# Performance work log

Measured on AMD Instinct MI355X. Metric: run time of the kernel, lower is better.

The kernel has to match this reference:

```python
import jax, jax.numpy as jnp
import numpy as np

B, D, R = 8192, 4096, 64
REG_W, REG_C = 0.01, 0.05


def setup_inputs() -> dict:
    key = jax.random.key(0)
    ks = jax.random.split(key, 7)
    return {
        "X": jax.random.normal(ks[0], (B, D), dtype=jnp.float32),
        "U1": jax.random.normal(ks[1], (1, D, R), dtype=jnp.float32),
        "U2": jax.random.normal(ks[2], (2, D, R), dtype=jnp.float32),
        "U3": jax.random.normal(ks[3], (3, D, R), dtype=jnp.float32),
        "C": jax.random.normal(ks[4], (3,), dtype=jnp.float32),
        "beta": jax.random.normal(ks[5], (1,), dtype=jnp.float32),
        "C_sin": jax.random.normal(ks[6], (1,), dtype=jnp.float32),
    }


def reference(X, U1, U2, U3, C, beta, C_sin):
    # term_j(x) = sum_r prod_{i<=j} <x, U_j[i, :, r]>
    result = jnp.broadcast_to(beta[0], (X.shape[0],))
    reg_loss_w = jnp.float32(0.0)
    for j, U in enumerate((U1, U2, U3)):
        dots = jnp.einsum("bd,odr->obr", X, U)      # [order, B, R]
        term = jnp.prod(dots, axis=0).sum(axis=1)   # [B]
        result = result + C[j] * term
        reg_loss_w = reg_loss_w + REG_W * (jnp.abs(U).sum() / U.size)
    sine_term = C_sin[0] * jnp.sin(X).sum(axis=1)
    result = result + sine_term
    reg_loss_c = REG_C * (jnp.abs(C).sum() + jnp.abs(C_sin).sum())
    total_reg = reg_loss_w + reg_loss_c
    return result, total_reg
```

## Files before the change

### kernel.cpp

```cpp
#include <hip/hip_runtime.h>
#include <hip/hip_bf16.h>

typedef float f32x4 __attribute__((ext_vector_type(4)));
typedef short s16x8 __attribute__((ext_vector_type(8)));

#define D_DIM 4096
#define NT 24
#define BM 128
#define NBODY 32
#define BOFF 0
#define AOFF 49152
#define SINW_OFF 3145728u
#define PART_OFF 3276800u

__device__ __forceinline__ unsigned short f2bf(float f) {
    unsigned u = __float_as_uint(f);
    u += 0x7fffu + ((u >> 16) & 1u);
    return (unsigned short)(u >> 16);
}

__device__ __forceinline__ void gload16(const void* g, void* l) {
    __builtin_amdgcn_global_load_lds(
        (const __attribute__((address_space(1))) unsigned int*)g,
        (__attribute__((address_space(3))) unsigned int*)l, 16, 0, 0);
}

__global__ __launch_bounds__(64) void reg_init_kernel(const float* __restrict__ C,
                                                      const float* __restrict__ Csin,
                                                      float* __restrict__ reg_out) {
    if (threadIdx.x == 0)
        reg_out[0] = 0.05f * (fabsf(C[0]) + fabsf(C[1]) + fabsf(C[2]) + fabsf(Csin[0]));
}

__global__ __launch_bounds__(64) void build_w_kernel(const float* __restrict__ U1,
                                                     const float* __restrict__ U2,
                                                     const float* __restrict__ U3,
                                                     unsigned short* __restrict__ W,
                                                     float* __restrict__ reg_out) {
    const int ks = blockIdx.x / NT;
    const int ct = blockIdx.x % NT;
    const int l  = threadIdx.x;
    const int n  = ct * 16 + (l & 15);
    const int kb = ks * 32 + ((l >> 4) << 3);

    const float* src;
    float scale;
    if (n < 64)       { src = U1 + n;                  scale = 0.01f / 262144.f; }
    else if (n < 128) { src = U2 + (n - 64);           scale = 0.01f / 524288.f; }
    else if (n < 192) { src = U2 + 262144 + (n - 128); scale = 0.01f / 524288.f; }
    else if (n < 256) { src = U3 + (n - 192);          scale = 0.01f / 786432.f; }
    else if (n < 320) { src = U3 + 262144 + (n - 256); scale = 0.01f / 786432.f; }
    else              { src = U3 + 524288 + (n - 320); scale = 0.01f / 786432.f; }

    unsigned short h[8];
    float sabs = 0.f;
#pragma unroll
    for (int j = 0; j < 8; ++j) {
        float u = src[(size_t)(kb + j) * 64];
        sabs += fabsf(u);
        h[j] = f2bf(u);
    }
    uint4 pk;
    pk.x = (unsigned)h[0] | ((unsigned)h[1] << 16);
    pk.y = (unsigned)h[2] | ((unsigned)h[3] << 16);
    pk.z = (unsigned)h[4] | ((unsigned)h[5] << 16);
    pk.w = (unsigned)h[6] | ((unsigned)h[7] << 16);
    *(uint4*)(W + ((size_t)blockIdx.x * 64 + l) * 8) = pk;

    sabs *= scale;
#pragma unroll
    for (int off = 32; off >= 1; off >>= 1)
        sabs += __shfl_xor(sabs, off, 64);
    if (l == 0) atomicAdd(reg_out, sabs);
}

__global__ __launch_bounds__(1024, 4) void poly_main_kernel(const float* __restrict__ X,
                                                            const unsigned short* __restrict__ W,
                                                            _Float16* __restrict__ part,
                                                            float* __restrict__ sinws) {
    __shared__ __align__(16) char pool[65536];

    const int t    = threadIdx.x;
    const int lane = t & 63;
    const int wv   = t >> 6;
    const int rg   = wv >> 3;
    const int cg   = wv & 7;
    const int ct0  = cg * 3;
    const int rb   = blockIdx.x >> 2;
    const int ks   = blockIdx.x & 3;
    const int row0 = rb * BM;

    const int sr = t >> 3;
    const int k4 = (t & 7) << 2;
    const float* xp = X + (size_t)(row0 + sr) * D_DIM + ks * 1024 + k4;
    const int awfrag = (sr >> 4) * 1024
                     + ((((k4 >> 3) << 4) | (sr & 15)) * 16) + ((k4 & 7) << 1);

    const int nB  = (wv < 8) ? 2 : 1;
    const int ch0 = (wv < 8) ? (wv * 2) : (wv + 8);
    const int slab0 = ks * 32;

    f32x4 acc00{}, acc01{}, acc02{}, acc10{}, acc11{}, acc12{},
          acc20{}, acc21{}, acc22{}, acc30{}, acc31{}, acc32{};
    float sinacc = 0.f;

#define STAGE(bufl, XV)                                                         \
    {                                                                           \
        sinacc += __sinf(XV.x) + __sinf(XV.y) + __sinf(XV.z) + __sinf(XV.w);    \
        uint2 h_;                                                               \
        h_.x = (unsigned)f2bf(XV.x) | ((unsigned)f2bf(XV.y) << 16);             \
        h_.y = (unsigned)f2bf(XV.z) | ((unsigned)f2bf(XV.w) << 16);             \
        *(uint2*)(pool + AOFF + (bufl) * 8192 + awfrag) = h_;                   \
    }

    {
        const unsigned short* g0 = W + (size_t)slab0 * 12288 + ch0 * 512 + lane * 8;
        gload16(g0, pool + BOFF + ch0 * 1024);
        if (nB == 2) gload16(g0 + 512, pool + BOFF + (ch0 + 1) * 1024);
    }
    f32x4 xn;
    {
        f32x4 x0 = *(const f32x4*)xp;
        STAGE(0, x0);
        xn = *(const f32x4*)(xp + 32);
    }
    asm volatile("s_waitcnt lgkmcnt(0)" ::: "memory");
    asm volatile("s_waitcnt vmcnt(1)" ::: "memory");
    __builtin_amdgcn_s_barrier();
    __builtin_amdgcn_sched_barrier(0);

#define BODY(d_, CUR, NXT)                                                      \
    {                                                                           \
        const int d__ = (d_);                                                   \
        if (d__ + 1 < NBODY) {                                                  \
            const unsigned short* g_ = W + (size_t)(slab0 + d__ + 1) * 12288    \
                                         + ch0 * 512 + lane * 8;                \
            gload16(g_, pool + BOFF + (NXT) * 24576 + ch0 * 1024);              \
            if (nB == 2)                                                        \
                gload16(g_ + 512, pool + BOFF + (NXT) * 24576 + (ch0 + 1) * 1024);\
        }                                                                       \
        int sl_ = d__ + 2; if (sl_ > NBODY - 1) sl_ = NBODY - 1;                \
        f32x4 xf_ = *(const f32x4*)(xp + (size_t)sl_ * 32);                     \
        if (d__ + 1 < NBODY) { STAGE(NXT, xn); }                                \
        xn = xf_;                                                               \
        const char* ab_ = pool + AOFF + (CUR) * 8192;                           \
        const char* bb_ = pool + BOFF + (CUR) * 24576;                          \
        s16x8 af0_ = *(const s16x8*)(ab_ + (rg * 4 + 0) * 1024 + lane * 16);    \
        s16x8 af1_ = *(const s16x8*)(ab_ + (rg * 4 + 1) * 1024 + lane * 16);    \
        s16x8 af2_ = *(const s16x8*)(ab_ + (rg * 4 + 2) * 1024 + lane * 16);    \
        s16x8 af3_ = *(const s16x8*)(ab_ + (rg * 4 + 3) * 1024 + lane * 16);    \
        s16x8 bf0_ = *(const s16x8*)(bb_ + (ct0 + 0) * 1024 + lane * 16);       \
        s16x8 bf1_ = *(const s16x8*)(bb_ + (ct0 + 1) * 1024 + lane * 16);       \
        s16x8 bf2_ = *(const s16x8*)(bb_ + (ct0 + 2) * 1024 + lane * 16);       \
        asm volatile("s_waitcnt lgkmcnt(0)" ::: "memory");                      \
        __builtin_amdgcn_sched_barrier(0);                                      \
        __builtin_amdgcn_s_setprio(1);                                          \
        acc00 = __builtin_amdgcn_mfma_f32_16x16x32_bf16(af0_, bf0_, acc00, 0, 0, 0); \
        acc01 = __builtin_amdgcn_mfma_f32_16x16x32_bf16(af0_, bf1_, acc01, 0, 0, 0); \
        acc02 = __builtin_amdgcn_mfma_f32_16x16x32_bf16(af0_, bf2_, acc02, 0, 0, 0); \
        acc10 = __builtin_amdgcn_mfma_f32_16x16x32_bf16(af1_, bf0_, acc10, 0, 0, 0); \
        acc11 = __builtin_amdgcn_mfma_f32_16x16x32_bf16(af1_, bf1_, acc11, 0, 0, 0); \
        acc12 = __builtin_amdgcn_mfma_f32_16x16x32_bf16(af1_, bf2_, acc12, 0, 0, 0); \
        acc20 = __builtin_amdgcn_mfma_f32_16x16x32_bf16(af2_, bf0_, acc20, 0, 0, 0); \
        acc21 = __builtin_amdgcn_mfma_f32_16x16x32_bf16(af2_, bf1_, acc21, 0, 0, 0); \
        acc22 = __builtin_amdgcn_mfma_f32_16x16x32_bf16(af2_, bf2_, acc22, 0, 0, 0); \
        acc30 = __builtin_amdgcn_mfma_f32_16x16x32_bf16(af3_, bf0_, acc30, 0, 0, 0); \
        acc31 = __builtin_amdgcn_mfma_f32_16x16x32_bf16(af3_, bf1_, acc31, 0, 0, 0); \
        acc32 = __builtin_amdgcn_mfma_f32_16x16x32_bf16(af3_, bf2_, acc32, 0, 0, 0); \
        __builtin_amdgcn_s_setprio(0);                                          \
        asm volatile("s_waitcnt vmcnt(1)" ::: "memory");                        \
        __builtin_amdgcn_s_barrier();                                           \
        __builtin_amdgcn_sched_barrier(0);                                      \
    }

    for (int d = 0; d < NBODY; d += 2) {
        BODY(d, 0, 1);
        BODY(d + 1, 1, 0);
    }
#undef BODY
#undef STAGE

    _Float16* pb = part + (size_t)ks * 8192 * 384;
    const int lr4 = (lane >> 4) << 2;
    const int lc  = lane & 15;
    const f32x4 accA[4][3] = {{acc00, acc01, acc02}, {acc10, acc11, acc12},
                              {acc20, acc21, acc22}, {acc30, acc31, acc32}};
#pragma unroll
    for (int rf = 0; rf < 4; ++rf)
#pragma unroll
        for (int c = 0; c < 3; ++c) {
            const int col = (ct0 + c) * 16 + lc;
#pragma unroll
            for (int i = 0; i < 4; ++i) {
                const int rl = rg * 64 + rf * 16 + lr4 + i;
                pb[(size_t)(row0 + rl) * 384 + col] = (_Float16)accA[rf][c][i];
            }
        }

    sinacc += __shfl_xor(sinacc, 1);
    sinacc += __shfl_xor(sinacc, 2);
    sinacc += __shfl_xor(sinacc, 4);
    if ((t & 7) == 0)
        sinws[(size_t)ks * 8192 + row0 + sr] = sinacc;
}

__global__ __launch_bounds__(512) void combine_kernel(const _Float16* __restrict__ part,
                                                      const float* __restrict__ sinws,
                                                      const float* __restrict__ C,
                                                      const float* __restrict__ beta,
                                                      const float* __restrict__ Csin,
                                                      float* __restrict__ out) {
    const int t   = threadIdx.x;
    const int row = blockIdx.x * 32 + (t >> 4);
    const int cc  = t & 15;
    const size_t rbase = (size_t)row * 384;

    float t1 = 0.f, t2 = 0.f, t3 = 0.f;
#pragma unroll
    for (int j = 0; j < 4; ++j) {
        const int c = j * 16 + cc;
        float a1 = 0.f, a2 = 0.f, b2 = 0.f, a3 = 0.f, b3 = 0.f, c3 = 0.f;
#pragma unroll
        for (int q = 0; q < 4; ++q) {
            const _Float16* p = part + (size_t)q * 8192 * 384 + rbase;
            a1 += (float)p[c];
            a2 += (float)p[64 + c];
            b2 += (float)p[128 + c];
            a3 += (float)p[192 + c];
            b3 += (float)p[256 + c];
            c3 += (float)p[320 + c];
        }
        t1 += a1;
        t2 += a2 * b2;
        t3 += a3 * b3 * c3;
    }
#pragma unroll
    for (int off = 1; off < 16; off <<= 1) {
        t1 += __shfl_xor(t1, off, 16);
        t2 += __shfl_xor(t2, off, 16);
        t3 += __shfl_xor(t3, off, 16);
    }
    if (cc == 0) {
        const float s = sinws[row] + sinws[8192 + row]
                      + sinws[2 * 8192 + row] + sinws[3 * 8192 + row];
        out[row] = beta[0] + C[0] * t1 + C[1] * t2 + C[2] * t3 + Csin[0] * s;
    }
}

extern "C" void kernel_launch(void* const* d_in, const int* in_sizes, int n_in,
                              void* d_out, int out_size, void* d_ws, size_t ws_size,
                              hipStream_t stream) {
    const float* X   = (const float*)d_in[0];
    const float* U1  = (const float*)d_in[1];
    const float* U2  = (const float*)d_in[2];
    const float* U3  = (const float*)d_in[3];
    const float* Cc  = (const float*)d_in[4];
    const float* bet = (const float*)d_in[5];
    const float* Cs  = (const float*)d_in[6];
    float* out = (float*)d_out;

    unsigned short* W = (unsigned short*)d_ws;
    float* sinws = (float*)((char*)d_ws + SINW_OFF);
    _Float16* part = (_Float16*)((char*)d_ws + PART_OFF);

    reg_init_kernel<<<1, 64, 0, stream>>>(Cc, Cs, out + 8192);
    build_w_kernel<<<128 * NT, 64, 0, stream>>>(U1, U2, U3, W, out + 8192);
    poly_main_kernel<<<256, 1024, 0, stream>>>(X, W, part, sinws);
    combine_kernel<<<256, 512, 0, stream>>>(part, sinws, Cc, bet, Cs, out);
}
```

Measured before the change: 98.03 us.

## Split main GEMM column range across two half-size blocks

```diff
diff --git a/kernel.cpp b/kernel.cpp
--- a/kernel.cpp
+++ b/kernel.cpp
@@ -9,7 +9,7 @@
 #define BM 128
 #define NBODY 32
 #define BOFF 0
-#define AOFF 49152
+#define AOFF 24576
 #define SINW_OFF 3145728u
 #define PART_OFF 3276800u
 
@@ -74,58 +74,67 @@
     if (l == 0) atomicAdd(reg_out, sabs);
 }
 
-__global__ __launch_bounds__(1024, 4) void poly_main_kernel(const float* __restrict__ X,
-                                                            const unsigned short* __restrict__ W,
-                                                            _Float16* __restrict__ part,
-                                                            float* __restrict__ sinws) {
-    __shared__ __align__(16) char pool[65536];
+__global__ __launch_bounds__(512, 4) void poly_main_kernel(const float* __restrict__ X,
+                                                           const unsigned short* __restrict__ W,
+                                                           _Float16* __restrict__ part,
+                                                           float* __restrict__ sinws) {
+    __shared__ __align__(16) char pool[40960];
 
     const int t    = threadIdx.x;
     const int lane = t & 63;
     const int wv   = t >> 6;
-    const int rg   = wv >> 3;
-    const int cg   = wv & 7;
+    const int rg   = wv >> 2;
+    const int cg   = wv & 3;
     const int ct0  = cg * 3;
-    const int rb   = blockIdx.x >> 2;
-    const int ks   = blockIdx.x & 3;
+    const int rb   = blockIdx.x >> 3;
+    const int cs   = (blockIdx.x >> 2) & 1;
+    const int kh   = blockIdx.x & 3;
     const int row0 = rb * BM;
-
-    const int sr = t >> 3;
-    const int k4 = (t & 7) << 2;
-    const float* xp = X + (size_t)(row0 + sr) * D_DIM + ks * 1024 + k4;
-    const int awfrag = (sr >> 4) * 1024
-                     + ((((k4 >> 3) << 4) | (sr & 15)) * 16) + ((k4 & 7) << 1);
-
-    const int nB  = (wv < 8) ? 2 : 1;
-    const int ch0 = (wv < 8) ? (wv * 2) : (wv + 8);
-    const int slab0 = ks * 32;
-
-    f32x4 acc00{}, acc01{}, acc02{}, acc10{}, acc11{}, acc12{},
-          acc20{}, acc21{}, acc22{}, acc30{}, acc31{}, acc32{};
+    const bool doSin = (cs == 0);
+
+    const int sr = t >> 2;
+    const int q  = t & 3;
+    const float* xp = X + (size_t)(row0 + sr) * D_DIM + kh * 1024 + q * 8;
+    const int awfrag = (sr >> 4) * 1024 + (((q << 4) | (sr & 15)) << 4);
+
+    const int nB  = (wv < 4) ? 2 : 1;
+    const int ch0 = (wv < 4) ? (wv * 2) : (4 + wv);
+    const int slab0 = kh * 32;
+    const unsigned short* wbase = W + (size_t)slab0 * 12288 + cs * 6144
+                                    + ch0 * 512 + lane * 8;
+
+    f32x4 acc[4][3];
+#pragma unroll
+    for (int r = 0; r < 4; ++r)
+#pragma unroll
+        for (int c = 0; c < 3; ++c) acc[r][c] = (f32x4){0.f, 0.f, 0.f, 0.f};
     float sinacc = 0.f;
-
-#define STAGE(bufl, XV)                                                         \
+    f32x4 xn0, xn1;
+
+#define STAGE(bufl, XA, XB)                                                     \
     {                                                                           \
-        sinacc += __sinf(XV.x) + __sinf(XV.y) + __sinf(XV.z) + __sinf(XV.w);    \
-        uint2 h_;                                                               \
-        h_.x = (unsigned)f2bf(XV.x) | ((unsigned)f2bf(XV.y) << 16);             \
-        h_.y = (unsigned)f2bf(XV.z) | ((unsigned)f2bf(XV.w) << 16);             \
-        *(uint2*)(pool + AOFF + (bufl) * 8192 + awfrag) = h_;                   \
-    }
-
+        if (doSin)                                                              \
+            sinacc += __sinf(XA.x) + __sinf(XA.y) + __sinf(XA.z) + __sinf(XA.w) \
+                    + __sinf(XB.x) + __sinf(XB.y) + __sinf(XB.z) + __sinf(XB.w);\
+        uint4 h_;                                                               \
+        h_.x = (unsigned)f2bf(XA.x) | ((unsigned)f2bf(XA.y) << 16);             \
+        h_.y = (unsigned)f2bf(XA.z) | ((unsigned)f2bf(XA.w) << 16);             \
+        h_.z = (unsigned)f2bf(XB.x) | ((unsigned)f2bf(XB.y) << 16);             \
+        h_.w = (unsigned)f2bf(XB.z) | ((unsigned)f2bf(XB.w) << 16);             \
+        *(uint4*)(pool + AOFF + (bufl) * 8192 + awfrag) = h_;                   \
+    }
+
+    gload16(wbase, pool + BOFF + ch0 * 1024);
+    if (nB == 2) gload16(wbase + 512, pool + BOFF + (ch0 + 1) * 1024);
     {
-        const unsigned short* g0 = W + (size_t)slab0 * 12288 + ch0 * 512 + lane * 8;
-        gload16(g0, pool + BOFF + ch0 * 1024);
-        if (nB == 2) gload16(g0 + 512, pool + BOFF + (ch0 + 1) * 1024);
-    }
-    f32x4 xn;
-    {
-        f32x4 x0 = *(const f32x4*)xp;
-        STAGE(0, x0);
-        xn = *(const f32x4*)(xp + 32);
+        f32x4 x00 = *(const f32x4*)xp;
+        f32x4 x01 = *(const f32x4*)(xp + 4);
+        STAGE(0, x00, x01);
+        xn0 = *(const f32x4*)(xp + 32);
+        xn1 = *(const f32x4*)(xp + 36);
     }
     asm volatile("s_waitcnt lgkmcnt(0)" ::: "memory");
-    asm volatile("s_waitcnt vmcnt(1)" ::: "memory");
+    asm volatile("s_waitcnt vmcnt(2)" ::: "memory");
     __builtin_amdgcn_s_barrier();
     __builtin_amdgcn_sched_barrier(0);
 
@@ -133,18 +142,18 @@
     {                                                                           \
         const int d__ = (d_);                                                   \
         if (d__ + 1 < NBODY) {                                                  \
-            const unsigned short* g_ = W + (size_t)(slab0 + d__ + 1) * 12288    \
-                                         + ch0 * 512 + lane * 8;                \
-            gload16(g_, pool + BOFF + (NXT) * 24576 + ch0 * 1024);              \
+            const unsigned short* g_ = wbase + (size_t)(d__ + 1) * 12288;       \
+            gload16(g_, pool + BOFF + (NXT) * 12288 + ch0 * 1024);              \
             if (nB == 2)                                                        \
-                gload16(g_ + 512, pool + BOFF + (NXT) * 24576 + (ch0 + 1) * 1024);\
+                gload16(g_ + 512, pool + BOFF + (NXT) * 12288 + (ch0 + 1) * 1024);\
         }                                                                       \
         int sl_ = d__ + 2; if (sl_ > NBODY - 1) sl_ = NBODY - 1;                \
-        f32x4 xf_ = *(const f32x4*)(xp + (size_t)sl_ * 32);                     \
-        if (d__ + 1 < NBODY) { STAGE(NXT, xn); }                                \
-        xn = xf_;                                                               \
+        f32x4 xf0_ = *(const f32x4*)(xp + (size_t)sl_ * 32);                    \
+        f32x4 xf1_ = *(const f32x4*)(xp + (size_t)sl_ * 32 + 4);                \
+        if (d__ + 1 < NBODY) { STAGE(NXT, xn0, xn1); }                          \
+        xn0 = xf0_; xn1 = xf1_;                                                 \
         const char* ab_ = pool + AOFF + (CUR) * 8192;                           \
-        const char* bb_ = pool + BOFF + (CUR) * 24576;                          \
+        const char* bb_ = pool + BOFF + (CUR) * 12288;                          \
         s16x8 af0_ = *(const s16x8*)(ab_ + (rg * 4 + 0) * 1024 + lane * 16);    \
         s16x8 af1_ = *(const s16x8*)(ab_ + (rg * 4 + 1) * 1024 + lane * 16);    \
         s16x8 af2_ = *(const s16x8*)(ab_ + (rg * 4 + 2) * 1024 + lane * 16);    \
@@ -155,20 +164,20 @@
         asm volatile("s_waitcnt lgkmcnt(0)" ::: "memory");                      \
         __builtin_amdgcn_sched_barrier(0);                                      \
         __builtin_amdgcn_s_setprio(1);                                          \
-        acc00 = __builtin_amdgcn_mfma_f32_16x16x32_bf16(af0_, bf0_, acc00, 0, 0, 0); \
-        acc01 = __builtin_amdgcn_mfma_f32_16x16x32_bf16(af0_, bf1_, acc01, 0, 0, 0); \
-        acc02 = __builtin_amdgcn_mfma_f32_16x16x32_bf16(af0_, bf2_, acc02, 0, 0, 0); \
-        acc10 = __builtin_amdgcn_mfma_f32_16x16x32_bf16(af1_, bf0_, acc10, 0, 0, 0); \
-        acc11 = __builtin_amdgcn_mfma_f32_16x16x32_bf16(af1_, bf1_, acc11, 0, 0, 0); \
-        acc12 = __builtin_amdgcn_mfma_f32_16x16x32_bf16(af1_, bf2_, acc12, 0, 0, 0); \
-        acc20 = __builtin_amdgcn_mfma_f32_16x16x32_bf16(af2_, bf0_, acc20, 0, 0, 0); \
-        acc21 = __builtin_amdgcn_mfma_f32_16x16x32_bf16(af2_, bf1_, acc21, 0, 0, 0); \
-        acc22 = __builtin_amdgcn_mfma_f32_16x16x32_bf16(af2_, bf2_, acc22, 0, 0, 0); \
-        acc30 = __builtin_amdgcn_mfma_f32_16x16x32_bf16(af3_, bf0_, acc30, 0, 0, 0); \
-        acc31 = __builtin_amdgcn_mfma_f32_16x16x32_bf16(af3_, bf1_, acc31, 0, 0, 0); \
-        acc32 = __builtin_amdgcn_mfma_f32_16x16x32_bf16(af3_, bf2_, acc32, 0, 0, 0); \
+        acc[0][0] = __builtin_amdgcn_mfma_f32_16x16x32_bf16(af0_, bf0_, acc[0][0], 0, 0, 0); \
+        acc[0][1] = __builtin_amdgcn_mfma_f32_16x16x32_bf16(af0_, bf1_, acc[0][1], 0, 0, 0); \
+        acc[0][2] = __builtin_amdgcn_mfma_f32_16x16x32_bf16(af0_, bf2_, acc[0][2], 0, 0, 0); \
+        acc[1][0] = __builtin_amdgcn_mfma_f32_16x16x32_bf16(af1_, bf0_, acc[1][0], 0, 0, 0); \
+        acc[1][1] = __builtin_amdgcn_mfma_f32_16x16x32_bf16(af1_, bf1_, acc[1][1], 0, 0, 0); \
+        acc[1][2] = __builtin_amdgcn_mfma_f32_16x16x32_bf16(af1_, bf2_, acc[1][2], 0, 0, 0); \
+        acc[2][0] = __builtin_amdgcn_mfma_f32_16x16x32_bf16(af2_, bf0_, acc[2][0], 0, 0, 0); \
+        acc[2][1] = __builtin_amdgcn_mfma_f32_16x16x32_bf16(af2_, bf1_, acc[2][1], 0, 0, 0); \
+        acc[2][2] = __builtin_amdgcn_mfma_f32_16x16x32_bf16(af2_, bf2_, acc[2][2], 0, 0, 0); \
+        acc[3][0] = __builtin_amdgcn_mfma_f32_16x16x32_bf16(af3_, bf0_, acc[3][0], 0, 0, 0); \
+        acc[3][1] = __builtin_amdgcn_mfma_f32_16x16x32_bf16(af3_, bf1_, acc[3][1], 0, 0, 0); \
+        acc[3][2] = __builtin_amdgcn_mfma_f32_16x16x32_bf16(af3_, bf2_, acc[3][2], 0, 0, 0); \
         __builtin_amdgcn_s_setprio(0);                                          \
-        asm volatile("s_waitcnt vmcnt(1)" ::: "memory");                        \
+        asm volatile("s_waitcnt vmcnt(2)" ::: "memory");                        \
         __builtin_amdgcn_s_barrier();                                           \
         __builtin_amdgcn_sched_barrier(0);                                      \
     }
@@ -180,28 +189,27 @@
 #undef BODY
 #undef STAGE
 
-    _Float16* pb = part + (size_t)ks * 8192 * 384;
+    _Float16* pb = part + (size_t)kh * 8192 * 384;
     const int lr4 = (lane >> 4) << 2;
     const int lc  = lane & 15;
-    const f32x4 accA[4][3] = {{acc00, acc01, acc02}, {acc10, acc11, acc12},
-                              {acc20, acc21, acc22}, {acc30, acc31, acc32}};
 #pragma unroll
     for (int rf = 0; rf < 4; ++rf)
 #pragma unroll
         for (int c = 0; c < 3; ++c) {
-            const int col = (ct0 + c) * 16 + lc;
+            const int col = cs * 192 + (ct0 + c) * 16 + lc;
 #pragma unroll
             for (int i = 0; i < 4; ++i) {
                 const int rl = rg * 64 + rf * 16 + lr4 + i;
-                pb[(size_t)(row0 + rl) * 384 + col] = (_Float16)accA[rf][c][i];
+                pb[(size_t)(row0 + rl) * 384 + col] = (_Float16)acc[rf][c][i];
             }
         }
 
-    sinacc += __shfl_xor(sinacc, 1);
-    sinacc += __shfl_xor(sinacc, 2);
-    sinacc += __shfl_xor(sinacc, 4);
-    if ((t & 7) == 0)
-        sinws[(size_t)ks * 8192 + row0 + sr] = sinacc;
+    if (doSin) {
+        sinacc += __shfl_xor(sinacc, 1);
+        sinacc += __shfl_xor(sinacc, 2);
+        if ((t & 3) == 0)
+            sinws[(size_t)kh * 8192 + row0 + sr] = sinacc;
+    }
 }
 
 __global__ __launch_bounds__(512) void combine_kernel(const _Float16* __restrict__ part,
@@ -221,8 +229,8 @@
         const int c = j * 16 + cc;
         float a1 = 0.f, a2 = 0.f, b2 = 0.f, a3 = 0.f, b3 = 0.f, c3 = 0.f;
 #pragma unroll
-        for (int q = 0; q < 4; ++q) {
-            const _Float16* p = part + (size_t)q * 8192 * 384 + rbase;
+        for (int qq = 0; qq < 4; ++qq) {
+            const _Float16* p = part + (size_t)qq * 8192 * 384 + rbase;
             a1 += (float)p[c];
             a2 += (float)p[64 + c];
             b2 += (float)p[128 + c];
@@ -265,6 +273,6 @@
 
     reg_init_kernel<<<1, 64, 0, stream>>>(Cc, Cs, out + 8192);
     build_w_kernel<<<128 * NT, 64, 0, stream>>>(U1, U2, U3, W, out + 8192);
-    poly_main_kernel<<<256, 1024, 0, stream>>>(X, W, part, sinws);
+    poly_main_kernel<<<512, 512, 0, stream>>>(X, W, part, sinws);
     combine_kernel<<<256, 512, 0, stream>>>(part, sinws, Cc, bet, Cs, out);
 }
```

Result: slower. 102.1 us (+4.1%).
